# Kernel tuning notes

Measured on AMD Instinct MI355X. Metric: run time of the kernel, lower is better.

Reference implementation:

```python
import jax, jax.numpy as jnp
import numpy as np

BATCH, SEQ, EMBED, HIDDEN, VOCAB = 32, 64, 512, 512, 32000

def setup_inputs() -> dict:
    key = jax.random.key(0)
    ks = jax.random.split(key, 11)
    s = lambda k, shape, scale: jax.random.normal(k, shape, dtype=jnp.float32) * scale
    return {
        "features": s(ks[0], (BATCH, HIDDEN), 1.0),
        "captions": jax.random.randint(ks[1], (BATCH, SEQ), 0, VOCAB),
        "embedding": s(ks[2], (VOCAB, EMBED), 1.0),
        "Wz_w": s(ks[3], (HIDDEN, EMBED + HIDDEN), 0.03),
        "Wz_b": s(ks[4], (HIDDEN,), 0.03),
        "Wr_w": s(ks[5], (HIDDEN, EMBED + HIDDEN), 0.03),
        "Wr_b": s(ks[6], (HIDDEN,), 0.03),
        "Wh_w": s(ks[7], (HIDDEN, EMBED + HIDDEN), 0.03),
        "Wh_b": s(ks[8], (HIDDEN,), 0.03),
        "fc_w": s(ks[9], (VOCAB, HIDDEN), 0.03),
        "fc_b": s(ks[10], (VOCAB,), 0.03),
    }

def reference(features, captions, embedding, Wz_w, Wz_b, Wr_w, Wr_b, Wh_w, Wh_b, fc_w, fc_b):
    # embeddings: [B, T, E] -> scan over time with xs [T, B, E]
    emb = embedding[captions]                      # [B, T, E]
    xs = jnp.swapaxes(emb, 0, 1)                   # [T, B, E]

    def step(h, x_t):
        comb = jnp.concatenate([x_t, h], axis=1)                   # [B, E+H]
        z = jax.nn.sigmoid(comb @ Wz_w.T + Wz_b)                   # update gate
        r = jax.nn.sigmoid(comb @ Wr_w.T + Wr_b)                   # reset gate
        comb_r = jnp.concatenate([x_t, r * h], axis=1)
        h_tilde = jnp.tanh(comb_r @ Wh_w.T + Wh_b)
        h_new = (1.0 - z) * h + z * h_tilde
        return h_new, h_new

    _, hs = jax.lax.scan(step, features, xs)       # hs: [T, B, H]
    hs = jnp.swapaxes(hs, 0, 1)                    # [B, T, H]
    # output projection done once over all timesteps (same math as per-step fc_out)
    logits = jnp.einsum('bth,vh->btv', hs, fc_w) + fc_b  # [B, T, V]
    return logits
```

## Files before the change

### kernel.cpp

```cpp
#include <hip/hip_runtime.h>
#include <hip/hip_bf16.h>

typedef __bf16 bf16;
typedef __bf16 bf16x8 __attribute__((ext_vector_type(8)));
typedef float f32x4 __attribute__((ext_vector_type(4)));
typedef unsigned int u32x4 __attribute__((ext_vector_type(4)));

#define B_SZ 32
#define T_SZ 64
#define H_SZ 512
#define V_SZ 32000
#define NWG_REC 8
#define NTILES 250
#define MTILES 16

__device__ __forceinline__ float sigmoidf_(float v) { return 1.0f / (1.0f + expf(-v)); }

__device__ __forceinline__ bf16x8 cvt8(const float* __restrict__ p) {
  float4 a = *(const float4*)p;
  float4 b = *(const float4*)(p + 4);
  bf16x8 o;
  o[0] = (bf16)a.x; o[1] = (bf16)a.y; o[2] = (bf16)a.z; o[3] = (bf16)a.w;
  o[4] = (bf16)b.x; o[5] = (bf16)b.y; o[6] = (bf16)b.z; o[7] = (bf16)b.w;
  return o;
}

#define GLD(dst, base, off) \
  asm volatile("global_load_dwordx4 %0, %1, off offset:" off " sc0 sc1" \
               : "=v"(dst) : "v"(base))
#define GST2(base, off, val) do { \
  unsigned int w_ = (unsigned int)__builtin_bit_cast(unsigned short, (bf16)(val)); \
  asm volatile("global_store_short %0, %1, off offset:" off " sc0 sc1" \
               :: "v"(base), "v"(w_) : "memory"); \
} while (0)
#define WAITV  asm volatile("s_waitcnt vmcnt(0)" ::: "memory")
#define SCHEDB __builtin_amdgcn_sched_barrier(0)

__device__ __forceinline__ int llc_poll(const int* p) {
  int r;
  asm volatile("global_load_dword %0, %1, off sc0 sc1\n\ts_waitcnt vmcnt(0)"
               : "=v"(r) : "v"(p) : "memory");
  return r;
}

__global__ __launch_bounds__(256) void xproj_k(
    const int* __restrict__ caps, const float* __restrict__ emb,
    const float* __restrict__ B0, const float* __restrict__ B1, const float* __restrict__ B2,
    const float* __restrict__ bias0, const float* __restrict__ bias1, const float* __restrict__ bias2,
    float* __restrict__ C, int gemm_blocks, int prep_start,
    const float* __restrict__ fcw_src, bf16* __restrict__ fcw_dst,
    const float* __restrict__ feat, bf16* __restrict__ hs, int* __restrict__ ctr,
    bf16* __restrict__ whp_dst)
{
  __shared__ __align__(16) bf16 lA[128 * 32];
  __shared__ __align__(16) bf16 lB[128 * 32];
  const int tid = threadIdx.x;
  const int bidx = blockIdx.x;

  if (bidx >= prep_start) {
    int i = (bidx - prep_start) * 256 + tid;
    int w = i >> 15;
    int rem = i & 32767;
    int n = rem >> 6;
    int k8 = (rem & 63) * 8;
    const float* W = (w == 0) ? B0 : (w == 1) ? B1 : B2;
    *(bf16x8*)(whp_dst + (long)w * 262144 + n * 512 + k8) = cvt8(W + (long)n * 1024 + 512 + k8);
    if (i < B_SZ * H_SZ) hs[i] = (bf16)feat[i];
    if (i < 128) ctr[i] = 0;
    return;
  }

  if (bidx >= gemm_blocks) {
    long base = ((long)(bidx - gemm_blocks) * 256 + tid) * 8;
    const long stride = (long)128 * 256 * 8;
    for (long i = base; i < (long)V_SZ * H_SZ; i += stride)
      *(bf16x8*)(fcw_dst + i) = cvt8(fcw_src + i);
    return;
  }

  const int lane = tid & 63;
  const int l15  = lane & 15;
  const int kb8  = (lane >> 4) * 8;
  const int wid  = tid >> 6;
  const int wm   = wid >> 1, wn = wid & 1;
  const int mtile = bidx % 16, ntile = bidx / 16;
  const int m0 = mtile * 128, n0 = ntile * 128;

  int wsel = n0 >> 9;
  const float* Bv   = wsel == 0 ? B0 : wsel == 1 ? B1 : B2;
  const float* bias = wsel == 0 ? bias0 : wsel == 1 ? bias1 : bias2;
  int nb = n0 & 511;

  f32x4 acc[4][4] = {};

  for (int k0 = 0; k0 < 512; k0 += 32) {
    #pragma unroll
    for (int j = 0; j < 2; ++j) {
      int c = j * 256 + tid;
      int row = c >> 2;
      int kc = (c & 3) * 8;
      *(bf16x8*)&lA[row * 32 + kc] = cvt8(emb + (long)caps[m0 + row] * 512 + k0 + kc);
      *(bf16x8*)&lB[row * 32 + kc] = cvt8(Bv + (long)(nb + row) * 1024 + k0 + kc);
    }
    __syncthreads();
    bf16x8 af[4], bfr[4];
    #pragma unroll
    for (int mf = 0; mf < 4; ++mf)
      af[mf] = *(const bf16x8*)&lA[(wm * 64 + mf * 16 + l15) * 32 + kb8];
    #pragma unroll
    for (int nf = 0; nf < 4; ++nf)
      bfr[nf] = *(const bf16x8*)&lB[(wn * 64 + nf * 16 + l15) * 32 + kb8];
    #pragma unroll
    for (int mf = 0; mf < 4; ++mf)
      #pragma unroll
      for (int nf = 0; nf < 4; ++nf)
        acc[mf][nf] = __builtin_amdgcn_mfma_f32_16x16x32_bf16(af[mf], bfr[nf], acc[mf][nf], 0, 0, 0);
    __syncthreads();
  }

  #pragma unroll
  for (int mf = 0; mf < 4; ++mf)
    #pragma unroll
    for (int nf = 0; nf < 4; ++nf)
      #pragma unroll
      for (int r = 0; r < 4; ++r) {
        int row = m0 + wm * 64 + mf * 16 + (lane >> 4) * 4 + r;
        int lc  = wn * 64 + nf * 16 + l15;
        C[(long)row * 1536 + n0 + lc] = acc[mf][nf][r] + bias[nb + lc];
      }
}

__global__ __launch_bounds__(512, 2) void fused_k(
    const float* __restrict__ X,
    const bf16* __restrict__ Wzh, const bf16* __restrict__ Wrh, const bf16* __restrict__ Whh,
    const float* __restrict__ feat,
    bf16* __restrict__ rh_g, bf16* __restrict__ hs, int* __restrict__ ctr,
    const bf16* __restrict__ fcw16, const float* __restrict__ fcw_f32,
    const float* __restrict__ fc_b, float* __restrict__ out, int use_bf16B)
{
  __shared__ __align__(16) char smem[20480];
  const int tid  = threadIdx.x;
  const int bid  = blockIdx.x;
  const int lane = tid & 63;
  const int l15  = lane & 15;

  if (bid < NWG_REC) {
    char* ldsb = smem;
    const int u    = bid * 8 + (tid >> 6);
    const int kb   = (lane >> 4) * 8;
    const int rq   = (lane >> 4) * 4;
    const int b0   = (u >> 5) * 16;
    const int gcol = (u & 31) * 16 + l15;
    const int grp  = bid >> 2;
    int* mctr  = ctr + grp * 32;
    int* progG = ctr + 64 + grp * 32;

    u32x4 Bz[16], Br[16], Bh[16];
    #pragma unroll
    for (int kk = 0; kk < 16; ++kk) {
      Bz[kk] = *(const u32x4*)(Wzh + (long)gcol * 512 + kk * 32 + kb);
      Br[kk] = *(const u32x4*)(Wrh + (long)gcol * 512 + kk * 32 + kb);
      Bh[kk] = *(const u32x4*)(Whh + (long)gcol * 512 + kk * 32 + kb);
    }
    #pragma unroll
    for (int kk = 0; kk < 16; ++kk)
      asm volatile("" : "+v"(Bz[kk]), "+v"(Br[kk]), "+v"(Bh[kk]));

    float hprev[4];
    #pragma unroll
    for (int r = 0; r < 4; ++r) hprev[r] = feat[(b0 + rq + r) * 512 + gcol];

    const float* xb = X + (long)(b0 + rq) * 64 * 1536 + gcol;
    float xz[4], xr[4];
    #pragma unroll
    for (int r = 0; r < 4; ++r) {
      xz[r] = xb[r * 98304];
      xr[r] = xb[r * 98304 + 512];
    }

    const int srow0 = tid >> 6;
    const int soff0 = (tid * 16) ^ ((srow0 & 7) << 4);
    const int soff1 = (8192 + tid * 16) ^ ((srow0 & 7) << 4);
    const int fbase = (l15 * 1024 + (lane >> 4) * 16) ^ ((l15 & 7) << 4);

    bf16* rhst = rh_g + (b0 + rq) * 512 + gcol;

    int epoch = 0;
    for (int t = 0; t < T_SZ; ++t) {
      {
        const bf16* src = hs + (long)(t * 32 + b0) * 512;
        u32x4 v0, v1;
        GLD(v0, src + tid * 8, "0");
        GLD(v1, src + 4096 + tid * 8, "0");
        WAITV;
        SCHEDB;
        *(u32x4*)(ldsb + soff0) = v0;
        *(u32x4*)(ldsb + soff1) = v1;
      }
      __syncthreads();
      f32x4 ze = {}, re = {};
      #pragma unroll
      for (int kk = 0; kk < 16; ++kk) {
        bf16x8 a = *(const bf16x8*)(ldsb + (fbase ^ (kk * 64)));
        ze = __builtin_amdgcn_mfma_f32_16x16x32_bf16(a, __builtin_bit_cast(bf16x8, Bz[kk]), ze, 0, 0, 0);
        re = __builtin_amdgcn_mfma_f32_16x16x32_bf16(a, __builtin_bit_cast(bf16x8, Br[kk]), re, 0, 0, 0);
      }
      float xh[4];
      #pragma unroll
      for (int r = 0; r < 4; ++r) xh[r] = xb[r * 98304 + t * 1536 + 1024];
      f32x4 zf;
      {
        float r0 = sigmoidf_(re[0] + xr[0]) * hprev[0];
        float r1 = sigmoidf_(re[1] + xr[1]) * hprev[1];
        float r2 = sigmoidf_(re[2] + xr[2]) * hprev[2];
        float r3 = sigmoidf_(re[3] + xr[3]) * hprev[3];
        GST2(rhst, "0", r0); GST2(rhst, "1024", r1); GST2(rhst, "2048", r2); GST2(rhst, "3072", r3);
        #pragma unroll
        for (int r = 0; r < 4; ++r) zf[r] = sigmoidf_(ze[r] + xz[r]);
      }
      ++epoch;
      WAITV;
      __syncthreads();
      if (tid == 0) {
        __hip_atomic_fetch_add(mctr, 1, __ATOMIC_RELAXED, __HIP_MEMORY_SCOPE_AGENT);
        while (__hip_atomic_load(mctr, __ATOMIC_RELAXED, __HIP_MEMORY_SCOPE_AGENT) < 4 * epoch)
          __builtin_amdgcn_s_sleep(1);
      }
      __syncthreads();

      {
        const bf16* src = rh_g + b0 * 512;
        u32x4 v0, v1;
        GLD(v0, src + tid * 8, "0");
        GLD(v1, src + 4096 + tid * 8, "0");
        WAITV;
        SCHEDB;
        *(u32x4*)(ldsb + soff0) = v0;
        *(u32x4*)(ldsb + soff1) = v1;
      }
      __syncthreads();
      f32x4 he = {};
      #pragma unroll
      for (int kk = 0; kk < 16; ++kk) {
        bf16x8 a = *(const bf16x8*)(ldsb + (fbase ^ (kk * 64)));
        he = __builtin_amdgcn_mfma_f32_16x16x32_bf16(a, __builtin_bit_cast(bf16x8, Bh[kk]), he, 0, 0, 0);
      }
      if (t + 1 < T_SZ) {
        #pragma unroll
        for (int r = 0; r < 4; ++r) {
          xz[r] = xb[r * 98304 + (t + 1) * 1536];
          xr[r] = xb[r * 98304 + (t + 1) * 1536 + 512];
        }
      }
      bf16* ph = hs + (long)((t + 1) * 32 + b0 + rq) * 512 + gcol;
      #pragma unroll
      for (int r = 0; r < 4; ++r) {
        float ht = tanhf(he[r] + xh[r]);
        float hn = hprev[r] + zf[r] * (ht - hprev[r]);
        hprev[r] = hn;
      }
      GST2(ph, "0", hprev[0]); GST2(ph, "1024", hprev[1]);
      GST2(ph, "2048", hprev[2]); GST2(ph, "3072", hprev[3]);
      ++epoch;
      WAITV;
      __syncthreads();
      if (tid == 0) {
        __hip_atomic_fetch_add(mctr, 1, __ATOMIC_RELAXED, __HIP_MEMORY_SCOPE_AGENT);
        while (__hip_atomic_load(mctr, __ATOMIC_RELAXED, __HIP_MEMORY_SCOPE_AGENT) < 4 * epoch)
          __builtin_amdgcn_s_sleep(1);
        if ((bid & 3) == 0) {
          int e = epoch;
          asm volatile("global_store_dword %0, %1, off sc0 sc1" :: "v"(progG), "v"(e) : "memory");
        }
      }
      __syncthreads();
    }
    return;
  }

  const int lwg   = bid - NWG_REC;
  const int mtile = lwg / NTILES;
  const int ntile = lwg % NTILES;
  const int m0 = mtile * 128, n0 = ntile * 128;

  if (tid < 2) {
    const int tgt = 8 * (mtile + 1);
    const int* p = ctr + 64 + tid * 32;
    while (llc_poll(p) < tgt) __builtin_amdgcn_s_sleep(32);
  }
  __syncthreads();

  const bf16* hsW = hs + 16384;
  bf16* lA = (bf16*)smem;
  bf16* lB = (bf16*)(smem + 10240);
  const int kb8  = (lane >> 4) * 8;
  const int wid  = tid >> 6;
  const int wm   = wid >> 1;
  const int wn   = wid & 1;
  const int arow = tid >> 2;
  const int akc  = (tid & 3) * 8;

  f32x4 acc[2][4] = {};

  for (int k0 = 0; k0 < 512; k0 += 32) {
    u32x4 av = *(const u32x4*)(hsW + (long)(m0 + arow) * 512 + k0 + akc);
    bf16x8 bv;
    if (use_bf16B) bv = *(const bf16x8*)(fcw16 + (long)(n0 + arow) * 512 + k0 + akc);
    else           bv = cvt8(fcw_f32 + (long)(n0 + arow) * 512 + k0 + akc);
    *(u32x4*)&lA[arow * 40 + akc] = av;
    *(bf16x8*)&lB[arow * 40 + akc] = bv;
    __syncthreads();
    bf16x8 af[2], bfr[4];
    #pragma unroll
    for (int mf = 0; mf < 2; ++mf)
      af[mf] = *(const bf16x8*)&lA[(wm * 32 + mf * 16 + l15) * 40 + kb8];
    #pragma unroll
    for (int nf = 0; nf < 4; ++nf)
      bfr[nf] = *(const bf16x8*)&lB[(wn * 64 + nf * 16 + l15) * 40 + kb8];
    #pragma unroll
    for (int mf = 0; mf < 2; ++mf)
      #pragma unroll
      for (int nf = 0; nf < 4; ++nf)
        acc[mf][nf] = __builtin_amdgcn_mfma_f32_16x16x32_bf16(af[mf], bfr[nf], acc[mf][nf], 0, 0, 0);
    __syncthreads();
  }

  #pragma unroll
  for (int mf = 0; mf < 2; ++mf)
    #pragma unroll
    for (int nf = 0; nf < 4; ++nf) {
      int col = n0 + wn * 64 + nf * 16 + l15;
      float bias_v = fc_b[col];
      #pragma unroll
      for (int r = 0; r < 4; ++r) {
        int rr = m0 + wm * 32 + mf * 16 + (lane >> 4) * 4 + r;
        int tt = rr >> 5, b = rr & 31;
        out[(long)(b * 64 + tt) * 32000 + col] = acc[mf][nf][r] + bias_v;
      }
    }
}

extern "C" void kernel_launch(void* const* d_in, const int* in_sizes, int n_in,
                              void* d_out, int out_size, void* d_ws, size_t ws_size,
                              hipStream_t stream) {
  const float* feat = (const float*)d_in[0];
  const int*   caps = (const int*)d_in[1];
  const float* emb  = (const float*)d_in[2];
  const float* Wz_w = (const float*)d_in[3];
  const float* Wz_b = (const float*)d_in[4];
  const float* Wr_w = (const float*)d_in[5];
  const float* Wr_b = (const float*)d_in[6];
  const float* Wh_w = (const float*)d_in[7];
  const float* Wh_b = (const float*)d_in[8];
  const float* fc_w = (const float*)d_in[9];
  const float* fc_b = (const float*)d_in[10];
  float* out = (float*)d_out;

  char* ws = (char*)d_ws;
  float* X_all = (float*)(ws + 0);
  bf16*  rh_g  = (bf16*) (ws + 12582912);
  bf16*  hs    = (bf16*) (ws + 12615680);
  bf16*  Whp   = (bf16*) (ws + 14745600);
  int*   ctr   = (int*)  (ws + 16318464);
  bf16*  fcw16 = (bf16*) (ws + 16318976);
  const bool cvt_fc = (ws_size >= (size_t)49087000);

  const int prep_start = cvt_fc ? 320 : 192;
  xproj_k<<<dim3(prep_start + 384), dim3(256), 0, stream>>>(
      caps, emb, Wz_w, Wr_w, Wh_w, Wz_b, Wr_b, Wh_b, X_all, 192, prep_start,
      fc_w, fcw16, feat, hs, ctr, Whp);

  fused_k<<<dim3(NWG_REC + MTILES * NTILES), dim3(512), 0, stream>>>(
      X_all, Whp, Whp + 262144, Whp + 524288, feat, rh_g, hs, ctr,
      fcw16, fc_w, fc_b, out, cvt_fc ? 1 : 0);
}
```

Measured before the change: 610.4 us.

## Compute reset gate redundantly per workgroup to remove mid-step grid barrier

Each recurrent workgroup now computes the full reset-gate product r*h for its 16-row batch group locally, streaming Wr from global memory each step, and keeps r*h in LDS. This removes the global rh buffer round-trip and one inter-workgroup atomic barrier per timestep. It also stops preloading the x projections into registers and lowers progress signalling to every fourth step, adjusting the consumer poll target to match. The cost is four times the Wr MFMA work per workgroup plus repeated global loads of Wr and X every step, and larger LDS.

```diff
diff --git a/kernel.cpp b/kernel.cpp
--- a/kernel.cpp
+++ b/kernel.cpp
@@ -134,56 +134,46 @@
     const float* __restrict__ X,
     const bf16* __restrict__ Wzh, const bf16* __restrict__ Wrh, const bf16* __restrict__ Whh,
     const float* __restrict__ feat,
-    bf16* __restrict__ rh_g, bf16* __restrict__ hs, int* __restrict__ ctr,
+    bf16* __restrict__ hs, int* __restrict__ ctr,
     const bf16* __restrict__ fcw16, const float* __restrict__ fcw_f32,
     const float* __restrict__ fc_b, float* __restrict__ out, int use_bf16B)
 {
-  __shared__ __align__(16) char smem[20480];
+  __shared__ __align__(16) char smem[32768];
   const int tid  = threadIdx.x;
   const int bid  = blockIdx.x;
   const int lane = tid & 63;
   const int l15  = lane & 15;
+  const int q    = lane >> 4;
 
   if (bid < NWG_REC) {
-    char* ldsb = smem;
-    const int u    = bid * 8 + (tid >> 6);
-    const int kb   = (lane >> 4) * 8;
-    const int rq   = (lane >> 4) * 4;
-    const int b0   = (u >> 5) * 16;
-    const int gcol = (u & 31) * 16 + l15;
+    char* h_lds  = smem;
+    char* rh_lds = smem + 16384;
+    const int wid  = tid >> 6;
+    const int kb   = q * 8;
     const int grp  = bid >> 2;
+    const int b0   = grp * 16;
+    const int ocol = (bid & 3) * 128 + wid * 16 + l15;
     int* mctr  = ctr + grp * 32;
     int* progG = ctr + 64 + grp * 32;
 
-    u32x4 Bz[16], Br[16], Bh[16];
+    u32x4 Bz[16], Bh[16];
     #pragma unroll
     for (int kk = 0; kk < 16; ++kk) {
-      Bz[kk] = *(const u32x4*)(Wzh + (long)gcol * 512 + kk * 32 + kb);
-      Br[kk] = *(const u32x4*)(Wrh + (long)gcol * 512 + kk * 32 + kb);
-      Bh[kk] = *(const u32x4*)(Whh + (long)gcol * 512 + kk * 32 + kb);
+      Bz[kk] = *(const u32x4*)(Wzh + (long)ocol * 512 + kk * 32 + kb);
+      Bh[kk] = *(const u32x4*)(Whh + (long)ocol * 512 + kk * 32 + kb);
     }
     #pragma unroll
     for (int kk = 0; kk < 16; ++kk)
-      asm volatile("" : "+v"(Bz[kk]), "+v"(Br[kk]), "+v"(Bh[kk]));
+      asm volatile("" : "+v"(Bz[kk]), "+v"(Bh[kk]));
 
     float hprev[4];
     #pragma unroll
-    for (int r = 0; r < 4; ++r) hprev[r] = feat[(b0 + rq + r) * 512 + gcol];
-
-    const float* xb = X + (long)(b0 + rq) * 64 * 1536 + gcol;
-    float xz[4], xr[4];
-    #pragma unroll
-    for (int r = 0; r < 4; ++r) {
-      xz[r] = xb[r * 98304];
-      xr[r] = xb[r * 98304 + 512];
-    }
+    for (int r = 0; r < 4; ++r) hprev[r] = feat[(b0 + q * 4 + r) * 512 + ocol];
 
     const int srow0 = tid >> 6;
     const int soff0 = (tid * 16) ^ ((srow0 & 7) << 4);
     const int soff1 = (8192 + tid * 16) ^ ((srow0 & 7) << 4);
-    const int fbase = (l15 * 1024 + (lane >> 4) * 16) ^ ((l15 & 7) << 4);
-
-    bf16* rhst = rh_g + (b0 + rq) * 512 + gcol;
+    const int fbase = (l15 * 1024 + q * 16) ^ ((l15 & 7) << 4);
 
     int epoch = 0;
     for (int t = 0; t < T_SZ; ++t) {
@@ -194,68 +184,54 @@
         GLD(v1, src + 4096 + tid * 8, "0");
         WAITV;
         SCHEDB;
-        *(u32x4*)(ldsb + soff0) = v0;
-        *(u32x4*)(ldsb + soff1) = v1;
+        *(u32x4*)(h_lds + soff0) = v0;
+        *(u32x4*)(h_lds + soff1) = v1;
       }
       __syncthreads();
-      f32x4 ze = {}, re = {};
+
+      f32x4 ze = {}, racc[4] = {};
       #pragma unroll
       for (int kk = 0; kk < 16; ++kk) {
-        bf16x8 a = *(const bf16x8*)(ldsb + (fbase ^ (kk * 64)));
+        bf16x8 a = *(const bf16x8*)(h_lds + (fbase ^ (kk * 64)));
         ze = __builtin_amdgcn_mfma_f32_16x16x32_bf16(a, __builtin_bit_cast(bf16x8, Bz[kk]), ze, 0, 0, 0);
-        re = __builtin_amdgcn_mfma_f32_16x16x32_bf16(a, __builtin_bit_cast(bf16x8, Br[kk]), re, 0, 0, 0);
-      }
-      float xh[4];
-      #pragma unroll
-      for (int r = 0; r < 4; ++r) xh[r] = xb[r * 98304 + t * 1536 + 1024];
+        #pragma unroll
+        for (int nf = 0; nf < 4; ++nf) {
+          u32x4 bw = *(const u32x4*)(Wrh + (long)(wid * 64 + nf * 16 + l15) * 512 + kk * 32 + kb);
+          racc[nf] = __builtin_amdgcn_mfma_f32_16x16x32_bf16(a, __builtin_bit_cast(bf16x8, bw), racc[nf], 0, 0, 0);
+        }
+      }
+      #pragma unroll
+      for (int nf = 0; nf < 4; ++nf) {
+        int col = wid * 64 + nf * 16 + l15;
+        #pragma unroll
+        for (int rr = 0; rr < 4; ++rr) {
+          int row = q * 4 + rr;
+          float xrv = X[(long)((b0 + row) * 64 + t) * 1536 + 512 + col];
+          float rv = sigmoidf_(racc[nf][rr] + xrv);
+          int byteoff = (row * 1024 + col * 2) ^ ((row & 7) << 4);
+          float hv = (float)*(const bf16*)(h_lds + byteoff);
+          *(bf16*)(rh_lds + byteoff) = (bf16)(rv * hv);
+        }
+      }
       f32x4 zf;
-      {
-        float r0 = sigmoidf_(re[0] + xr[0]) * hprev[0];
-        float r1 = sigmoidf_(re[1] + xr[1]) * hprev[1];
-        float r2 = sigmoidf_(re[2] + xr[2]) * hprev[2];
-        float r3 = sigmoidf_(re[3] + xr[3]) * hprev[3];
-        GST2(rhst, "0", r0); GST2(rhst, "1024", r1); GST2(rhst, "2048", r2); GST2(rhst, "3072", r3);
-        #pragma unroll
-        for (int r = 0; r < 4; ++r) zf[r] = sigmoidf_(ze[r] + xz[r]);
-      }
-      ++epoch;
-      WAITV;
+      #pragma unroll
+      for (int r = 0; r < 4; ++r) {
+        float xzv = X[(long)((b0 + q * 4 + r) * 64 + t) * 1536 + ocol];
+        zf[r] = sigmoidf_(ze[r] + xzv);
+      }
       __syncthreads();
-      if (tid == 0) {
-        __hip_atomic_fetch_add(mctr, 1, __ATOMIC_RELAXED, __HIP_MEMORY_SCOPE_AGENT);
-        while (__hip_atomic_load(mctr, __ATOMIC_RELAXED, __HIP_MEMORY_SCOPE_AGENT) < 4 * epoch)
-          __builtin_amdgcn_s_sleep(1);
-      }
-      __syncthreads();
-
-      {
-        const bf16* src = rh_g + b0 * 512;
-        u32x4 v0, v1;
-        GLD(v0, src + tid * 8, "0");
-        GLD(v1, src + 4096 + tid * 8, "0");
-        WAITV;
-        SCHEDB;
-        *(u32x4*)(ldsb + soff0) = v0;
-        *(u32x4*)(ldsb + soff1) = v1;
-      }
-      __syncthreads();
+
       f32x4 he = {};
       #pragma unroll
       for (int kk = 0; kk < 16; ++kk) {
-        bf16x8 a = *(const bf16x8*)(ldsb + (fbase ^ (kk * 64)));
+        bf16x8 a = *(const bf16x8*)(rh_lds + (fbase ^ (kk * 64)));
         he = __builtin_amdgcn_mfma_f32_16x16x32_bf16(a, __builtin_bit_cast(bf16x8, Bh[kk]), he, 0, 0, 0);
       }
-      if (t + 1 < T_SZ) {
-        #pragma unroll
-        for (int r = 0; r < 4; ++r) {
-          xz[r] = xb[r * 98304 + (t + 1) * 1536];
-          xr[r] = xb[r * 98304 + (t + 1) * 1536 + 512];
-        }
-      }
-      bf16* ph = hs + (long)((t + 1) * 32 + b0 + rq) * 512 + gcol;
+      bf16* ph = hs + (long)((t + 1) * 32 + b0 + q * 4) * 512 + ocol;
       #pragma unroll
       for (int r = 0; r < 4; ++r) {
-        float ht = tanhf(he[r] + xh[r]);
+        float xhv = X[(long)((b0 + q * 4 + r) * 64 + t) * 1536 + 1024 + ocol];
+        float ht = tanhf(he[r] + xhv);
         float hn = hprev[r] + zf[r] * (ht - hprev[r]);
         hprev[r] = hn;
       }
@@ -268,7 +244,7 @@
         __hip_atomic_fetch_add(mctr, 1, __ATOMIC_RELAXED, __HIP_MEMORY_SCOPE_AGENT);
         while (__hip_atomic_load(mctr, __ATOMIC_RELAXED, __HIP_MEMORY_SCOPE_AGENT) < 4 * epoch)
           __builtin_amdgcn_s_sleep(1);
-        if ((bid & 3) == 0) {
+        if ((bid & 3) == 0 && (t & 3) == 3) {
           int e = epoch;
           asm volatile("global_store_dword %0, %1, off sc0 sc1" :: "v"(progG), "v"(e) : "memory");
         }
@@ -284,7 +260,7 @@
   const int m0 = mtile * 128, n0 = ntile * 128;
 
   if (tid < 2) {
-    const int tgt = 8 * (mtile + 1);
+    const int tgt = 4 * (mtile + 1);
     const int* p = ctr + 64 + tid * 32;
     while (llc_poll(p) < tgt) __builtin_amdgcn_s_sleep(32);
   }
@@ -293,7 +269,7 @@
   const bf16* hsW = hs + 16384;
   bf16* lA = (bf16*)smem;
   bf16* lB = (bf16*)(smem + 10240);
-  const int kb8  = (lane >> 4) * 8;
+  const int kb8  = q * 8;
   const int wid  = tid >> 6;
   const int wm   = wid >> 1;
   const int wn   = wid & 1;
@@ -333,7 +309,7 @@
       float bias_v = fc_b[col];
       #pragma unroll
       for (int r = 0; r < 4; ++r) {
-        int rr = m0 + wm * 32 + mf * 16 + (lane >> 4) * 4 + r;
+        int rr = m0 + wm * 32 + mf * 16 + q * 4 + r;
         int tt = rr >> 5, b = rr & 31;
         out[(long)(b * 64 + tt) * 32000 + col] = acc[mf][nf][r] + bias_v;
       }
@@ -358,8 +334,7 @@
 
   char* ws = (char*)d_ws;
   float* X_all = (float*)(ws + 0);
-  bf16*  rh_g  = (bf16*) (ws + 12582912);
-  bf16*  hs    = (bf16*) (ws + 12615680);
+  bf16*  hs    = (bf16*) (ws + 12582912);
   bf16*  Whp   = (bf16*) (ws + 14745600);
   int*   ctr   = (int*)  (ws + 16318464);
   bf16*  fcw16 = (bf16*) (ws + 16318976);
@@ -371,6 +346,6 @@
       fc_w, fcw16, feat, hs, ctr, Whp);
 
   fused_k<<<dim3(NWG_REC + MTILES * NTILES), dim3(512), 0, stream>>>(
-      X_all, Whp, Whp + 262144, Whp + 524288, feat, rh_g, hs, ctr,
+      X_all, Whp, Whp + 262144, Whp + 524288, feat, hs, ctr,
       fcw16, fc_w, fc_b, out, cvt_fc ? 1 : 0);
 }
```

Measured after the change: 1.741 ms. 185% more time.
